# Kernel optimization log

Measured on AMD Instinct MI355X. Metric: run time of the kernel, lower is better.

The kernel has to match this reference:

```python
import jax, jax.numpy as jnp
import numpy as np

N_NODES = 100000
N_EDGES = 3200000
N_IN = 5
N_OUT = 16


def setup_inputs() -> dict:
    key = jax.random.key(0)
    k1, k2, k3, k4 = jax.random.split(key, 4)
    atom = jax.random.normal(k1, (N_NODES, N_IN), dtype=jnp.float32)
    edge_index = jax.random.randint(k2, (2, N_EDGES), 0, N_NODES, dtype=jnp.int64)
    # Linear(n_input=5, n_neural=16) parameters
    W = jax.random.normal(k3, (N_OUT, N_IN), dtype=jnp.float32) / np.sqrt(N_IN)
    b = jax.random.normal(k4, (N_OUT,), dtype=jnp.float32) * 0.01
    return {"atom": atom, "edge_index": edge_index, "W": W, "b": b}


def reference(atom, edge_index, W, b):
    n = atom.shape[0]
    # add_self_loops
    loops = jnp.arange(n, dtype=edge_index.dtype)
    row = jnp.concatenate([edge_index[0], loops])  # source nodes [E+N]
    col = jnp.concatenate([edge_index[1], loops])  # target nodes [E+N]
    # x = Linear(atom)
    x = atom @ W.T + b  # [N, n_out]
    # degree over target index (includes self loops -> deg >= 1)
    deg = jax.ops.segment_sum(jnp.ones_like(col, dtype=x.dtype), col, num_segments=n)
    dis = deg ** -0.5  # deg_inv_sqrt, finite since deg >= 1
    norm = dis[row] * dis[col]  # [E+N]
    # gather-scale-scatter: message = norm * x_j, aggr='add' at col
    msgs = norm[:, None] * x[row]  # [E+N, n_out]
    out = jax.ops.segment_sum(msgs, col, num_segments=n)  # [N, n_out]
    return jax.nn.relu(out)
```

## Files before the change

### kernel.cpp

```cpp
#include <hip/hip_runtime.h>

#define N_IN 5
#define N_OUT 16
#define NB 50
#define BN 2048
#define CAP 66560
#define MAXSUB 8
#define QSCALE 2048.0f
#define QBIAS 16384

__global__ void init_cursor(int* __restrict__ cursor) {
    if (threadIdx.x < NB) cursor[threadIdx.x] = threadIdx.x * CAP;
}

__global__ __launch_bounds__(1024) void partition_kernel(
        const int* __restrict__ row, const int* __restrict__ col,
        int e, int* __restrict__ eb, int* __restrict__ cursor) {
    __shared__ int hist[NB];
    __shared__ int base[NB];
    __shared__ int lofs[NB];
    int e4 = e >> 2;
    int nchunk = (e4 + 1023) / 1024;
    const int4* rowv = (const int4*)row;
    const int4* colv = (const int4*)col;
    for (int ch = blockIdx.x; ch < nchunk; ch += gridDim.x) {
        int i = ch * 1024 + threadIdx.x;
        bool valid = i < e4;
        int rr[4], cc[4], bb[4];
        if (valid) {
            int4 r4 = rowv[i];
            int4 c4 = colv[i];
            rr[0] = r4.x; rr[1] = r4.y; rr[2] = r4.z; rr[3] = r4.w;
            cc[0] = c4.x; cc[1] = c4.y; cc[2] = c4.z; cc[3] = c4.w;
        }
        if (threadIdx.x < NB) { hist[threadIdx.x] = 0; lofs[threadIdx.x] = 0; }
        __syncthreads();
        if (valid) {
#pragma unroll
            for (int j = 0; j < 4; ++j) {
                bb[j] = cc[j] >> 11;
                atomicAdd(&hist[bb[j]], 1);
            }
        }
        __syncthreads();
        if (threadIdx.x < NB) {
            int h = hist[threadIdx.x];
            base[threadIdx.x] = h ? atomicAdd(&cursor[threadIdx.x], h) : 0;
        }
        __syncthreads();
        if (valid) {
#pragma unroll
            for (int j = 0; j < 4; ++j) {
                int p = base[bb[j]] + atomicAdd(&lofs[bb[j]], 1);
                if (p < (bb[j] + 1) * CAP)
                    eb[p] = ((cc[j] & (BN - 1)) << 17) | rr[j];
            }
        }
        __syncthreads();
    }
    if (blockIdx.x == 0) {
        for (int i = (e4 << 2) + (int)threadIdx.x; i < e; i += (int)blockDim.x) {
            int c = col[i];
            int b = c >> 11;
            int p = atomicAdd(&cursor[b], 1);
            if (p < (b + 1) * CAP)
                eb[p] = ((c & (BN - 1)) << 17) | row[i];
        }
    }
}

__global__ __launch_bounds__(1024) void degcount(
        const int* __restrict__ eb, const int* __restrict__ cursor,
        unsigned short* __restrict__ degp, int nsub) {
    __shared__ int hist[BN];
    int bin = blockIdx.x / nsub;
    int sub = blockIdx.x % nsub;
    for (int j = threadIdx.x; j < BN; j += 1024) hist[j] = 0;
    __syncthreads();
    int s0 = bin * CAP;
    int cnt = min(max(cursor[bin] - s0, 0), CAP);
    int chunk = (cnt + nsub - 1) / nsub;
    int start = min(sub * chunk, cnt);
    int end = min(start + chunk, cnt);
    for (int i = s0 + start + (int)threadIdx.x; i < s0 + end; i += 1024)
        atomicAdd(&hist[eb[i] >> 17], 1);
    __syncthreads();
    unsigned short* dst = degp + (size_t)blockIdx.x * BN;
    for (int j = threadIdx.x; j < BN; j += 1024) dst[j] = (unsigned short)hist[j];
}

__global__ void dis_datom(const unsigned short* __restrict__ degp,
                          const float* __restrict__ atom,
                          float* __restrict__ dis_arr,
                          ulonglong2* __restrict__ datom, int n, int nsub) {
    int i = blockIdx.x * blockDim.x + threadIdx.x;
    if (i >= n) return;
    int bin = i >> 11;
    int l = i & (BN - 1);
    int deg = 0;
    for (int sb = 0; sb < nsub; ++sb)
        deg += degp[(size_t)(bin * nsub + sb) * BN + l];
    float d = rsqrtf((float)(deg + 1));
    dis_arr[i] = d;
    const float* ap = atom + (size_t)i * N_IN;
    unsigned long long f[6];
#pragma unroll
    for (int k = 0; k < 5; ++k) {
        int q = __float2int_rn(d * ap[k] * QSCALE);
        q = min(max(q, -16383), 16383);
        f[k] = (unsigned long long)(q + QBIAS);
    }
    {
        int q = __float2int_rn(d * QSCALE);
        f[5] = (unsigned long long)(q + QBIAS);
    }
    ulonglong2 v;
    v.x = f[0] | (f[1] << 21) | (f[2] << 42);
    v.y = f[3] | (f[4] << 21) | (f[5] << 42);
    datom[i] = v;
}

__global__ __launch_bounds__(1024) void accum_bin(
        const int* __restrict__ eb, const int* __restrict__ cursor,
        const ulonglong2* __restrict__ datom,
        const unsigned short* __restrict__ degp,
        float* __restrict__ accp, int nsub) {
    __shared__ unsigned long long accA[BN];
    __shared__ unsigned long long accB[BN];
    int bin = blockIdx.x / nsub;
    int sub = blockIdx.x % nsub;
    for (int j = threadIdx.x; j < BN; j += 1024) { accA[j] = 0ull; accB[j] = 0ull; }
    __syncthreads();
    int s0 = bin * CAP;
    int cnt = min(max(cursor[bin] - s0, 0), CAP);
    int chunk = (cnt + nsub - 1) / nsub;
    int start = min(sub * chunk, cnt);
    int end = min(start + chunk, cnt);
    int i = s0 + start + (int)threadIdx.x;
    int iend = s0 + end;
    for (; i + 1024 < iend; i += 2048) {
        int v0 = eb[i];
        int v1 = eb[i + 1024];
        ulonglong2 d0 = datom[v0 & 0x1FFFF];
        ulonglong2 d1 = datom[v1 & 0x1FFFF];
        int l0 = v0 >> 17;
        int l1 = v1 >> 17;
        atomicAdd(&accA[l0], d0.x);
        atomicAdd(&accB[l0], d0.y);
        atomicAdd(&accA[l1], d1.x);
        atomicAdd(&accB[l1], d1.y);
    }
    if (i < iend) {
        int v0 = eb[i];
        ulonglong2 d0 = datom[v0 & 0x1FFFF];
        int l0 = v0 >> 17;
        atomicAdd(&accA[l0], d0.x);
        atomicAdd(&accB[l0], d0.y);
    }
    __syncthreads();
    const unsigned short* dp = degp + (size_t)blockIdx.x * BN;
    float* dst = accp + (size_t)blockIdx.x * (6 * BN);
    const float inv = 1.0f / QSCALE;
    for (int j = threadIdx.x; j < BN; j += 1024) {
        unsigned long long SA = accA[j], SB = accB[j];
        int c = dp[j];
        int cb = c * QBIAS;
        dst[0 * BN + j] = (float)((int)((SA      ) & 0x1FFFFF) - cb) * inv;
        dst[1 * BN + j] = (float)((int)((SA >> 21) & 0x1FFFFF) - cb) * inv;
        dst[2 * BN + j] = (float)((int)((SA >> 42) & 0x1FFFFF) - cb) * inv;
        dst[3 * BN + j] = (float)((int)((SB      ) & 0x1FFFFF) - cb) * inv;
        dst[4 * BN + j] = (float)((int)((SB >> 21) & 0x1FFFFF) - cb) * inv;
        dst[5 * BN + j] = (float)((int)((SB >> 42) & 0x1FFFFF) - cb) * inv;
    }
}

__global__ void final_kernel(const float* __restrict__ accp,
                             const float* __restrict__ dis_arr,
                             const float* __restrict__ atom,
                             const float* __restrict__ W, const float* __restrict__ b,
                             float* __restrict__ out, int n, int nsub) {
    int i = blockIdx.x * blockDim.x + threadIdx.x;
    if (i >= n) return;
    int bin = i >> 11;
    int l = i & (BN - 1);
    float s[6] = {0.f, 0.f, 0.f, 0.f, 0.f, 0.f};
    for (int sb = 0; sb < nsub; ++sb) {
        const float* p = accp + (size_t)(bin * nsub + sb) * (6 * BN) + l;
#pragma unroll
        for (int k = 0; k < 6; ++k) s[k] += p[k * BN];
    }
    float d = dis_arr[i];
    const float* ap = atom + (size_t)i * N_IN;
    float t5[5];
#pragma unroll
    for (int k = 0; k < 5; ++k) t5[k] = d * (s[k] + d * ap[k]);
    float t1 = d * (s[5] + d);
    float ov[N_OUT];
#pragma unroll
    for (int o = 0; o < N_OUT; ++o) {
        float a = b[o] * t1;
#pragma unroll
        for (int k = 0; k < 5; ++k) a = fmaf(W[o * N_IN + k], t5[k], a);
        ov[o] = fmaxf(a, 0.0f);
    }
    float4* op = (float4*)(out + (size_t)i * N_OUT);
#pragma unroll
    for (int q = 0; q < 4; ++q)
        op[q] = make_float4(ov[4 * q], ov[4 * q + 1], ov[4 * q + 2], ov[4 * q + 3]);
}

extern "C" void kernel_launch(void* const* d_in, const int* in_sizes, int n_in,
                              void* d_out, int out_size, void* d_ws, size_t ws_size,
                              hipStream_t stream) {
    const float* atom = (const float*)d_in[0];
    const int*   eidx = (const int*)d_in[1];
    const float* W    = (const float*)d_in[2];
    const float* b    = (const float*)d_in[3];
    float* out = (float*)d_out;

    int n = in_sizes[0] / N_IN;
    int e = in_sizes[1] / 2;
    const int* row = eidx;
    const int* col = eidx + e;

    auto align256 = [](size_t v) { return (v + 255) & ~(size_t)255; };
    char* w = (char*)d_ws;
    int*        cursor = (int*)w;             w += align256(NB * 4);
    float*      dis    = (float*)w;           w += align256((size_t)n * 4);
    ulonglong2* datom  = (ulonglong2*)w;      w += align256((size_t)n * 16);
    int*        eb     = (int*)w;             w += align256((size_t)NB * CAP * 4);
    size_t fixed = (size_t)(w - (char*)d_ws);

    size_t per_sub = (size_t)NB * BN * 2 + (size_t)NB * 6 * BN * 4;
    int nsub = MAXSUB;
    if (ws_size > fixed) {
        size_t fit = (ws_size - fixed) / per_sub;
        if (fit < (size_t)nsub) nsub = (int)fit;
    } else nsub = 1;
    if (nsub < 1) nsub = 1;

    unsigned short* degp = (unsigned short*)w;
    w += align256((size_t)NB * nsub * BN * 2);
    float* accp = (float*)w;

    const int B = 256;
    init_cursor<<<1, 64, 0, stream>>>(cursor);
    partition_kernel<<<256, 1024, 0, stream>>>(row, col, e, eb, cursor);
    degcount<<<NB * nsub, 1024, 0, stream>>>(eb, cursor, degp, nsub);
    dis_datom<<<(n + B - 1) / B, B, 0, stream>>>(degp, atom, dis, datom, n, nsub);
    accum_bin<<<NB * nsub, 1024, 0, stream>>>(eb, cursor, datom, degp, accp, nsub);
    final_kernel<<<(n + B - 1) / B, B, 0, stream>>>(accp, dis, atom, W, b, out, n, nsub);
}
```

Baseline: 136.3 us.

## Fuse degree counting into partition, rebin to 64 bins, defer dequantization

Removes the separate degcount kernel by counting degrees with global atomics inside the partition pass, and drops the dis array by recomputing rsqrt in the final kernel. Bins change to 64 bins of 1600 nodes using a multiply-shift bin index, with a fixed 4-way split per bin. accum_bin now writes raw packed 64-bit partial sums, and final_kernel unpacks and dequantizes them, which cuts accumulator write traffic. In exchange, partition now issues per-edge global atomics on the degree array and loads int2 instead of int4 vectors, and the fixed split gives fewer accum blocks.

After: 250.6 us. 83.9% more time.

```diff
diff --git a/kernel.cpp b/kernel.cpp
--- a/kernel.cpp
+++ b/kernel.cpp
@@ -2,44 +2,52 @@
 
 #define N_IN 5
 #define N_OUT 16
-#define NB 50
-#define BN 2048
-#define CAP 66560
-#define MAXSUB 8
+#define NB 64
+#define BN 1600
+#define CAP 53248
+#define NSUB 4
 #define QSCALE 2048.0f
 #define QBIAS 16384
 
-__global__ void init_cursor(int* __restrict__ cursor) {
-    if (threadIdx.x < NB) cursor[threadIdx.x] = threadIdx.x * CAP;
+__device__ __forceinline__ int bin_of(int c) {
+    return (int)(((unsigned long long)(unsigned)c * 2684355ull) >> 32);
+}
+
+__global__ void init_kernel(int* __restrict__ deg, int n, int* __restrict__ cursor) {
+    int i = blockIdx.x * blockDim.x + threadIdx.x;
+    if (i < n) deg[i] = 0;
+    if (i < NB) cursor[i] = i * CAP;
 }
 
 __global__ __launch_bounds__(1024) void partition_kernel(
         const int* __restrict__ row, const int* __restrict__ col,
-        int e, int* __restrict__ eb, int* __restrict__ cursor) {
+        int e, int* __restrict__ eb, int* __restrict__ cursor,
+        int* __restrict__ deg) {
     __shared__ int hist[NB];
     __shared__ int base[NB];
     __shared__ int lofs[NB];
-    int e4 = e >> 2;
-    int nchunk = (e4 + 1023) / 1024;
-    const int4* rowv = (const int4*)row;
-    const int4* colv = (const int4*)col;
+    int e2 = e >> 1;
+    int nchunk = (e2 + 1023) / 1024;
+    const int2* rowv = (const int2*)row;
+    const int2* colv = (const int2*)col;
     for (int ch = blockIdx.x; ch < nchunk; ch += gridDim.x) {
         int i = ch * 1024 + threadIdx.x;
-        bool valid = i < e4;
-        int rr[4], cc[4], bb[4];
+        bool valid = i < e2;
+        int rr[2], cc[2], bb[2];
         if (valid) {
-            int4 r4 = rowv[i];
-            int4 c4 = colv[i];
-            rr[0] = r4.x; rr[1] = r4.y; rr[2] = r4.z; rr[3] = r4.w;
-            cc[0] = c4.x; cc[1] = c4.y; cc[2] = c4.z; cc[3] = c4.w;
+            int2 r2 = rowv[i];
+            int2 c2 = colv[i];
+            rr[0] = r2.x; rr[1] = r2.y;
+            cc[0] = c2.x; cc[1] = c2.y;
         }
         if (threadIdx.x < NB) { hist[threadIdx.x] = 0; lofs[threadIdx.x] = 0; }
         __syncthreads();
         if (valid) {
 #pragma unroll
-            for (int j = 0; j < 4; ++j) {
-                bb[j] = cc[j] >> 11;
+            for (int j = 0; j < 2; ++j) {
+                bb[j] = bin_of(cc[j]);
                 atomicAdd(&hist[bb[j]], 1);
+                atomicAdd(&deg[cc[j]], 1);
             }
         }
         __syncthreads();
@@ -50,58 +58,30 @@
         __syncthreads();
         if (valid) {
 #pragma unroll
-            for (int j = 0; j < 4; ++j) {
+            for (int j = 0; j < 2; ++j) {
                 int p = base[bb[j]] + atomicAdd(&lofs[bb[j]], 1);
-                if (p < (bb[j] + 1) * CAP)
-                    eb[p] = ((cc[j] & (BN - 1)) << 17) | rr[j];
+                if (p < (bb[j] + 1) * CAP) {
+                    int l = cc[j] - bb[j] * BN;
+                    eb[p] = (l << 17) | rr[j];
+                }
             }
         }
         __syncthreads();
     }
-    if (blockIdx.x == 0) {
-        for (int i = (e4 << 2) + (int)threadIdx.x; i < e; i += (int)blockDim.x) {
-            int c = col[i];
-            int b = c >> 11;
-            int p = atomicAdd(&cursor[b], 1);
-            if (p < (b + 1) * CAP)
-                eb[p] = ((c & (BN - 1)) << 17) | row[i];
-        }
-    }
-}
-
-__global__ __launch_bounds__(1024) void degcount(
-        const int* __restrict__ eb, const int* __restrict__ cursor,
-        unsigned short* __restrict__ degp, int nsub) {
-    __shared__ int hist[BN];
-    int bin = blockIdx.x / nsub;
-    int sub = blockIdx.x % nsub;
-    for (int j = threadIdx.x; j < BN; j += 1024) hist[j] = 0;
-    __syncthreads();
-    int s0 = bin * CAP;
-    int cnt = min(max(cursor[bin] - s0, 0), CAP);
-    int chunk = (cnt + nsub - 1) / nsub;
-    int start = min(sub * chunk, cnt);
-    int end = min(start + chunk, cnt);
-    for (int i = s0 + start + (int)threadIdx.x; i < s0 + end; i += 1024)
-        atomicAdd(&hist[eb[i] >> 17], 1);
-    __syncthreads();
-    unsigned short* dst = degp + (size_t)blockIdx.x * BN;
-    for (int j = threadIdx.x; j < BN; j += 1024) dst[j] = (unsigned short)hist[j];
-}
-
-__global__ void dis_datom(const unsigned short* __restrict__ degp,
-                          const float* __restrict__ atom,
-                          float* __restrict__ dis_arr,
-                          ulonglong2* __restrict__ datom, int n, int nsub) {
+    if (blockIdx.x == 0 && threadIdx.x == 0 && (e & 1)) {
+        int c = col[e - 1];
+        int b = bin_of(c);
+        atomicAdd(&deg[c], 1);
+        int p = atomicAdd(&cursor[b], 1);
+        if (p < (b + 1) * CAP) eb[p] = ((c - b * BN) << 17) | row[e - 1];
+    }
+}
+
+__global__ void dis_datom(const int* __restrict__ deg, const float* __restrict__ atom,
+                          ulonglong2* __restrict__ datom, int n) {
     int i = blockIdx.x * blockDim.x + threadIdx.x;
     if (i >= n) return;
-    int bin = i >> 11;
-    int l = i & (BN - 1);
-    int deg = 0;
-    for (int sb = 0; sb < nsub; ++sb)
-        deg += degp[(size_t)(bin * nsub + sb) * BN + l];
-    float d = rsqrtf((float)(deg + 1));
-    dis_arr[i] = d;
+    float d = rsqrtf((float)(deg[i] + 1));
     const float* ap = atom + (size_t)i * N_IN;
     unsigned long long f[6];
 #pragma unroll
@@ -110,10 +90,7 @@
         q = min(max(q, -16383), 16383);
         f[k] = (unsigned long long)(q + QBIAS);
     }
-    {
-        int q = __float2int_rn(d * QSCALE);
-        f[5] = (unsigned long long)(q + QBIAS);
-    }
+    f[5] = (unsigned long long)(__float2int_rn(d * QSCALE) + QBIAS);
     ulonglong2 v;
     v.x = f[0] | (f[1] << 21) | (f[2] << 42);
     v.y = f[3] | (f[4] << 21) | (f[5] << 42);
@@ -123,17 +100,16 @@
 __global__ __launch_bounds__(1024) void accum_bin(
         const int* __restrict__ eb, const int* __restrict__ cursor,
         const ulonglong2* __restrict__ datom,
-        const unsigned short* __restrict__ degp,
-        float* __restrict__ accp, int nsub) {
+        ulonglong2* __restrict__ accp) {
     __shared__ unsigned long long accA[BN];
     __shared__ unsigned long long accB[BN];
-    int bin = blockIdx.x / nsub;
-    int sub = blockIdx.x % nsub;
+    int bin = blockIdx.x >> 2;
+    int sub = blockIdx.x & 3;
     for (int j = threadIdx.x; j < BN; j += 1024) { accA[j] = 0ull; accB[j] = 0ull; }
     __syncthreads();
     int s0 = bin * CAP;
     int cnt = min(max(cursor[bin] - s0, 0), CAP);
-    int chunk = (cnt + nsub - 1) / nsub;
+    int chunk = (cnt + NSUB - 1) / NSUB;
     int start = min(sub * chunk, cnt);
     int end = min(start + chunk, cnt);
     int i = s0 + start + (int)threadIdx.x;
@@ -158,38 +134,40 @@
         atomicAdd(&accB[l0], d0.y);
     }
     __syncthreads();
-    const unsigned short* dp = degp + (size_t)blockIdx.x * BN;
-    float* dst = accp + (size_t)blockIdx.x * (6 * BN);
-    const float inv = 1.0f / QSCALE;
+    ulonglong2* dst = accp + (size_t)blockIdx.x * BN;
     for (int j = threadIdx.x; j < BN; j += 1024) {
-        unsigned long long SA = accA[j], SB = accB[j];
-        int c = dp[j];
-        int cb = c * QBIAS;
-        dst[0 * BN + j] = (float)((int)((SA      ) & 0x1FFFFF) - cb) * inv;
-        dst[1 * BN + j] = (float)((int)((SA >> 21) & 0x1FFFFF) - cb) * inv;
-        dst[2 * BN + j] = (float)((int)((SA >> 42) & 0x1FFFFF) - cb) * inv;
-        dst[3 * BN + j] = (float)((int)((SB      ) & 0x1FFFFF) - cb) * inv;
-        dst[4 * BN + j] = (float)((int)((SB >> 21) & 0x1FFFFF) - cb) * inv;
-        dst[5 * BN + j] = (float)((int)((SB >> 42) & 0x1FFFFF) - cb) * inv;
-    }
-}
-
-__global__ void final_kernel(const float* __restrict__ accp,
-                             const float* __restrict__ dis_arr,
+        ulonglong2 v; v.x = accA[j]; v.y = accB[j];
+        dst[j] = v;
+    }
+}
+
+__global__ void final_kernel(const ulonglong2* __restrict__ accp,
+                             const int* __restrict__ deg,
                              const float* __restrict__ atom,
                              const float* __restrict__ W, const float* __restrict__ b,
-                             float* __restrict__ out, int n, int nsub) {
+                             float* __restrict__ out, int n) {
     int i = blockIdx.x * blockDim.x + threadIdx.x;
     if (i >= n) return;
-    int bin = i >> 11;
-    int l = i & (BN - 1);
-    float s[6] = {0.f, 0.f, 0.f, 0.f, 0.f, 0.f};
-    for (int sb = 0; sb < nsub; ++sb) {
-        const float* p = accp + (size_t)(bin * nsub + sb) * (6 * BN) + l;
-#pragma unroll
-        for (int k = 0; k < 6; ++k) s[k] += p[k * BN];
-    }
-    float d = dis_arr[i];
+    int bin = bin_of(i);
+    int l = i - bin * BN;
+    int f[6] = {0, 0, 0, 0, 0, 0};
+#pragma unroll
+    for (int sb = 0; sb < NSUB; ++sb) {
+        ulonglong2 v = accp[(size_t)(bin * NSUB + sb) * BN + l];
+        f[0] += (int)(v.x & 0x1FFFFF);
+        f[1] += (int)((v.x >> 21) & 0x1FFFFF);
+        f[2] += (int)((v.x >> 42) & 0x1FFFFF);
+        f[3] += (int)(v.y & 0x1FFFFF);
+        f[4] += (int)((v.y >> 21) & 0x1FFFFF);
+        f[5] += (int)((v.y >> 42) & 0x1FFFFF);
+    }
+    int dg = deg[i];
+    int db = dg * QBIAS;
+    const float inv = 1.0f / QSCALE;
+    float s[6];
+#pragma unroll
+    for (int k = 0; k < 6; ++k) s[k] = (float)(f[k] - db) * inv;
+    float d = rsqrtf((float)(dg + 1));
     const float* ap = atom + (size_t)i * N_IN;
     float t5[5];
 #pragma unroll
@@ -225,29 +203,17 @@
 
     auto align256 = [](size_t v) { return (v + 255) & ~(size_t)255; };
     char* w = (char*)d_ws;
-    int*        cursor = (int*)w;             w += align256(NB * 4);
-    float*      dis    = (float*)w;           w += align256((size_t)n * 4);
-    ulonglong2* datom  = (ulonglong2*)w;      w += align256((size_t)n * 16);
-    int*        eb     = (int*)w;             w += align256((size_t)NB * CAP * 4);
-    size_t fixed = (size_t)(w - (char*)d_ws);
-
-    size_t per_sub = (size_t)NB * BN * 2 + (size_t)NB * 6 * BN * 4;
-    int nsub = MAXSUB;
-    if (ws_size > fixed) {
-        size_t fit = (ws_size - fixed) / per_sub;
-        if (fit < (size_t)nsub) nsub = (int)fit;
-    } else nsub = 1;
-    if (nsub < 1) nsub = 1;
-
-    unsigned short* degp = (unsigned short*)w;
-    w += align256((size_t)NB * nsub * BN * 2);
-    float* accp = (float*)w;
+    int*        cursor = (int*)w;        w += align256(NB * 4);
+    int*        deg    = (int*)w;        w += align256((size_t)n * 4);
+    ulonglong2* datom  = (ulonglong2*)w; w += align256((size_t)n * 16);
+    int*        eb     = (int*)w;        w += align256((size_t)NB * CAP * 4);
+    ulonglong2* accp   = (ulonglong2*)w;
 
     const int B = 256;
-    init_cursor<<<1, 64, 0, stream>>>(cursor);
-    partition_kernel<<<256, 1024, 0, stream>>>(row, col, e, eb, cursor);
-    degcount<<<NB * nsub, 1024, 0, stream>>>(eb, cursor, degp, nsub);
-    dis_datom<<<(n + B - 1) / B, B, 0, stream>>>(degp, atom, dis, datom, n, nsub);
-    accum_bin<<<NB * nsub, 1024, 0, stream>>>(eb, cursor, datom, degp, accp, nsub);
-    final_kernel<<<(n + B - 1) / B, B, 0, stream>>>(accp, dis, atom, W, b, out, n, nsub);
-}
+    int gn = (n + B - 1) / B;
+    init_kernel<<<gn, B, 0, stream>>>(deg, n, cursor);
+    partition_kernel<<<256, 1024, 0, stream>>>(row, col, e, eb, cursor, deg);
+    dis_datom<<<gn, B, 0, stream>>>(deg, atom, datom, n);
+    accum_bin<<<NB * NSUB, 1024, 0, stream>>>(eb, cursor, datom, accp);
+    final_kernel<<<gn, B, 0, stream>>>(accp, deg, atom, W, b, out, n);
+}
```
